# Performance work log

Measured on AMD Instinct MI355X. Metric: run time of the kernel, lower is better.

Reference implementation:

```python
import jax, jax.numpy as jnp
import numpy as np

JUMP_THRESHOLD = 0.5
BLEND = 0.7  # blend_factor in original


def _phase_corrected(x):
    # x: [B, C, T], C even; first half channels = magnitude, second = normalized phase
    half = x.shape[1] // 2
    magnitude = x[:, :half]
    phase_norm = x[:, half:]

    # phase_grad[t] = phase[t] - phase[t-1], with grad[0] = 0 (as in torch code)
    grad = jnp.concatenate(
        [jnp.zeros_like(phase_norm[:, :, :1]), phase_norm[:, :, 1:] - phase_norm[:, :, :-1]],
        axis=2,
    )
    jumps = jnp.abs(grad) > JUMP_THRESHOLD
    # The original O(T) python loop subtracts sign(grad[j]) from all positions >= j+1
    # whenever jumps[j]; equivalently a right-shifted cumulative sum of corrections.
    d = jnp.where(jumps, jnp.sign(grad), jnp.zeros_like(grad))
    corr = jnp.cumsum(d, axis=2)
    corr = jnp.concatenate([jnp.zeros_like(corr[:, :, :1]), corr[:, :, :-1]], axis=2)
    phase_smooth = phase_norm - corr

    phase = phase_smooth * (2.0 * jnp.pi) - jnp.pi

    # F.avg_pool1d(kernel=3, stride=1, padding=1) with count_include_pad=True:
    # zero-pad and divide by 3 everywhere (including edges).
    p = jnp.pad(phase, ((0, 0), (0, 0), (1, 1)))
    phase_smoothed = (p[:, :, :-2] + p[:, :, 1:-1] + p[:, :, 2:]) * (1.0 / 3.0)

    phase_final = BLEND * phase + (1.0 - BLEND) * phase_smoothed
    real_part = magnitude * jnp.cos(phase_final)
    imag_part = magnitude * jnp.sin(phase_final)
    return real_part, imag_part


def setup_inputs() -> dict:
    key = jax.random.key(0)
    x = jax.random.normal(key, (16, 128, 16384), dtype=jnp.float32)
    return {"x": x}


def reference(x):
    real_part, imag_part = _phase_corrected(x)
    return jax.lax.complex(real_part, imag_part)
```

## Files before the change

kernel.cpp:

```cpp
#include <hip/hip_runtime.h>
#include <math.h>

#define N_T   16384
#define BLOCK 1024
#define SEG   (N_T / BLOCK)
#define NWAVE (BLOCK / 64)

__device__ __forceinline__ int SW(int i) {
    return i ^ (((i >> 6) & 7) << 2);
}

template <int MODE>
__global__ __launch_bounds__(BLOCK)
void phase_kernel(const float* __restrict__ x, float* __restrict__ out) {
    __shared__ float ph[N_T];

    const int tid  = threadIdx.x;
    const int lane = tid & 63;
    const int wave = tid >> 6;
    const int r    = blockIdx.x;
    const int b    = r >> 6;
    const int c    = r & 63;
    const float* __restrict__ phase_row = x + ((size_t)(b * 128 + 64 + c)) * N_T;
    const float* __restrict__ mag_row   = x + ((size_t)(b * 128 + c)) * N_T;

    const float TWO_PI = 6.28318530717958647692f;
    const float PI_F   = 3.14159265358979323846f;
    const float THIRD  = 1.0f / 3.0f;

    #pragma unroll
    for (int i = 0; i < N_T / (BLOCK * 4); ++i) {
        int idx = (i * BLOCK + tid) * 4;
        float4 v = *reinterpret_cast<const float4*>(phase_row + idx);
        *reinterpret_cast<float4*>(&ph[SW(idx)]) = v;
    }
    __syncthreads();

    const int seg0 = tid * SEG;
    float s[SEG];
    #pragma unroll
    for (int q = 0; q < SEG / 4; ++q) {
        float4 v = *reinterpret_cast<const float4*>(&ph[SW(seg0 + q * 4)]);
        s[q * 4 + 0] = v.x; s[q * 4 + 1] = v.y;
        s[q * 4 + 2] = v.z; s[q * 4 + 3] = v.w;
    }
    float prevseg = __shfl_up(s[SEG - 1], 1);
    if (lane == 0) prevseg = (tid > 0) ? ph[SW(seg0 - 1)] : 0.0f;

    int lsum = 0;
    {
        float prev = prevseg;
        #pragma unroll
        for (int j = 0; j < SEG; ++j) {
            float g = s[j] - prev;
            if ((seg0 + j) > 0 && fabsf(g) > 0.5f) lsum += (g > 0.0f) ? 1 : -1;
            prev = s[j];
        }
    }

    int incl = lsum;
    #pragma unroll
    for (int off = 1; off < 64; off <<= 1) {
        int n = __shfl_up(incl, off);
        if (lane >= off) incl += n;
    }
    float saved;
    if (tid < NWAVE) saved = ph[tid];
    __syncthreads();
    if (lane == 63) ph[wave] = __int_as_float(incl);
    __syncthreads();
    int wpre = 0;
    #pragma unroll
    for (int w = 0; w < NWAVE; ++w) {
        int wt = __float_as_int(ph[w]);
        if (w < wave) wpre += wt;
    }
    __syncthreads();
    if (tid < NWAVE) ph[tid] = saved;
    __syncthreads();

    int running = wpre + incl - lsum;

    {
        float prev = prevseg;
        #pragma unroll
        for (int j = 0; j < SEG; ++j) {
            float cur = s[j];
            int d = 0;
            if ((seg0 + j) > 0) {
                float g = cur - prev;
                if (fabsf(g) > 0.5f) d = (g > 0.0f) ? 1 : -1;
            }
            s[j] = (cur - (float)running) * TWO_PI - PI_F;
            running += d;
            prev = cur;
        }
    }
    #pragma unroll
    for (int q = 0; q < SEG / 4; ++q) {
        *reinterpret_cast<float4*>(&ph[SW(seg0 + q * 4)]) =
            make_float4(s[q * 4 + 0], s[q * 4 + 1], s[q * 4 + 2], s[q * 4 + 3]);
    }
    __syncthreads();

    #pragma unroll
    for (int i = 0; i < N_T / (BLOCK * 4); ++i) {
        int e = (i * BLOCK + tid) * 4;
        float4 mg = *reinterpret_cast<const float4*>(mag_row + e);
        float4 pc = *reinterpret_cast<const float4*>(&ph[SW(e)]);

        float p_m1 = __shfl_up(pc.w, 1);
        if (lane == 0)  p_m1 = (e > 0) ? ph[SW(e - 1)] : 0.0f;
        float p_p4 = __shfl_down(pc.x, 1);
        if (lane == 63) p_p4 = (e + 4 < N_T) ? ph[SW(e + 4)] : 0.0f;

        float pv[6] = {p_m1, pc.x, pc.y, pc.z, pc.w, p_p4};
        float mgk[4] = {mg.x, mg.y, mg.z, mg.w};

        float re[4], im[4];
        #pragma unroll
        for (int k = 0; k < 4; ++k) {
            float sm = ((pv[k] + pv[k + 1]) + pv[k + 2]) * THIRD;
            float pf = 0.7f * pv[k + 1] + 0.3f * sm;
            float nrev = rintf(pf * 0.15915494309189535f);
            float rr = fmaf(nrev, -6.28318548202514648f, pf);
            rr = fmaf(nrev, 1.74845553e-7f, rr);
            re[k] = mgk[k] * __cosf(rr);
            if (MODE == 1) im[k] = mgk[k] * __sinf(rr);
        }
        if (MODE == 0) {
            float* orow = out + (size_t)r * N_T;
            *reinterpret_cast<float4*>(orow + e) = make_float4(re[0], re[1], re[2], re[3]);
        } else {
            float* orow = out + (size_t)r * (2 * N_T);
            *reinterpret_cast<float4*>(orow + 2 * e) =
                make_float4(re[0], im[0], re[1], im[1]);
            *reinterpret_cast<float4*>(orow + 2 * e + 4) =
                make_float4(re[2], im[2], re[3], im[3]);
        }
    }
}

extern "C" void kernel_launch(void* const* d_in, const int* in_sizes, int n_in,
                              void* d_out, int out_size, void* d_ws, size_t ws_size,
                              hipStream_t stream) {
    const float* x = (const float*)d_in[0];
    float* out = (float*)d_out;
    int n_rows = in_sizes[0] / (2 * N_T);
    if (out_size >= in_sizes[0]) {
        phase_kernel<1><<<n_rows, BLOCK, 0, stream>>>(x, out);
    } else {
        phase_kernel<0><<<n_rows, BLOCK, 0, stream>>>(x, out);
    }
}
```

Before: 39.13 us.

## Split each row's scan into chunks with a separate chunk-sum pre-pass kernel

Replaces the single 1024-thread block per row with a two-kernel decoupled scan. A first kernel counts phase jumps for each 4096-element chunk and stores the counts in workspace. The main kernel then runs 256-thread blocks per chunk, adds the counts of earlier chunks as an offset, and reconstructs the corrected boundary neighbours needed by the pooling. This gives four times as many smaller blocks for better occupancy and load balance, and it shrinks shared memory per block. The cost is a second launch and an extra full read of the phase data.

```diff
diff --git a/kernel.cpp b/kernel.cpp
--- a/kernel.cpp
+++ b/kernel.cpp
@@ -2,35 +2,84 @@
 #include <math.h>
 
 #define N_T   16384
-#define BLOCK 1024
-#define SEG   (N_T / BLOCK)
-#define NWAVE (BLOCK / 64)
+#define CHUNK 4096
+#define SEG   16
+#define CPR   4
 
 __device__ __forceinline__ int SW(int i) {
     return i ^ (((i >> 6) & 7) << 2);
 }
 
+__global__ __launch_bounds__(256)
+void chunk_sum_kernel(const float* __restrict__ x, int* __restrict__ ws) {
+    const int c    = blockIdx.x;
+    const int row  = c >> 2;
+    const int cpos = c & 3;
+    const int b    = row >> 6;
+    const int ch   = row & 63;
+    const float* __restrict__ pr =
+        x + ((size_t)(b * 128 + 64 + ch)) * N_T + cpos * CHUNK;
+    const int lane = threadIdx.x & 63;
+    const int wv   = threadIdx.x >> 6;
+    const float* __restrict__ wb = pr + wv * 1024;
+
+    float carry = 0.0f;
+    if (lane == 0 && !(cpos == 0 && wv == 0)) carry = wb[-1];
+    carry = __shfl(carry, 0);
+
+    int lsum = 0;
+    #pragma unroll
+    for (int i = 0; i < 4; ++i) {
+        float4 v = *reinterpret_cast<const float4*>(wb + i * 256 + lane * 4);
+        float up   = __shfl_up(v.w, 1);
+        float prev = (lane == 0) ? carry : up;
+        float g0 = v.x - prev;
+        float g1 = v.y - v.x;
+        float g2 = v.z - v.y;
+        float g3 = v.w - v.z;
+        bool first = (cpos == 0 && wv == 0 && i == 0 && lane == 0);
+        if (!first && fabsf(g0) > 0.5f) lsum += (g0 > 0.0f) ? 1 : -1;
+        if (fabsf(g1) > 0.5f)           lsum += (g1 > 0.0f) ? 1 : -1;
+        if (fabsf(g2) > 0.5f)           lsum += (g2 > 0.0f) ? 1 : -1;
+        if (fabsf(g3) > 0.5f)           lsum += (g3 > 0.0f) ? 1 : -1;
+        carry = __shfl(v.w, 63);
+    }
+    #pragma unroll
+    for (int off = 32; off; off >>= 1) lsum += __shfl_xor(lsum, off);
+
+    __shared__ int ws4[4];
+    if (lane == 0) ws4[wv] = lsum;
+    __syncthreads();
+    if (threadIdx.x == 0) ws[c] = ws4[0] + ws4[1] + ws4[2] + ws4[3];
+}
+
 template <int MODE>
-__global__ __launch_bounds__(BLOCK)
-void phase_kernel(const float* __restrict__ x, float* __restrict__ out) {
-    __shared__ float ph[N_T];
+__global__ __launch_bounds__(256)
+void phase_kernel(const float* __restrict__ x, float* __restrict__ out,
+                  const int* __restrict__ ws) {
+    __shared__ float ph[CHUNK];
+    __shared__ int   wsum[4];
 
     const int tid  = threadIdx.x;
     const int lane = tid & 63;
-    const int wave = tid >> 6;
-    const int r    = blockIdx.x;
-    const int b    = r >> 6;
-    const int c    = r & 63;
-    const float* __restrict__ phase_row = x + ((size_t)(b * 128 + 64 + c)) * N_T;
-    const float* __restrict__ mag_row   = x + ((size_t)(b * 128 + c)) * N_T;
+    const int wv   = tid >> 6;
+    const int c    = blockIdx.x;
+    const int row  = c >> 2;
+    const int cpos = c & 3;
+    const int b    = row >> 6;
+    const int ch   = row & 63;
+    const float* __restrict__ phase_row =
+        x + ((size_t)(b * 128 + 64 + ch)) * N_T + cpos * CHUNK;
+    const float* __restrict__ mag_row =
+        x + ((size_t)(b * 128 + ch)) * N_T + cpos * CHUNK;
 
     const float TWO_PI = 6.28318530717958647692f;
     const float PI_F   = 3.14159265358979323846f;
     const float THIRD  = 1.0f / 3.0f;
 
     #pragma unroll
-    for (int i = 0; i < N_T / (BLOCK * 4); ++i) {
-        int idx = (i * BLOCK + tid) * 4;
+    for (int i = 0; i < 4; ++i) {
+        int idx = (i * 256 + tid) * 4;
         float4 v = *reinterpret_cast<const float4*>(phase_row + idx);
         *reinterpret_cast<float4*>(&ph[SW(idx)]) = v;
     }
@@ -45,7 +94,11 @@
         s[q * 4 + 2] = v.z; s[q * 4 + 3] = v.w;
     }
     float prevseg = __shfl_up(s[SEG - 1], 1);
-    if (lane == 0) prevseg = (tid > 0) ? ph[SW(seg0 - 1)] : 0.0f;
+    if (lane == 0) {
+        if (tid > 0)            prevseg = ph[SW(seg0 - 1)];
+        else if (cpos > 0)      prevseg = phase_row[-1];
+        else                    prevseg = 0.0f;
+    }
 
     int lsum = 0;
     {
@@ -53,7 +106,8 @@
         #pragma unroll
         for (int j = 0; j < SEG; ++j) {
             float g = s[j] - prev;
-            if ((seg0 + j) > 0 && fabsf(g) > 0.5f) lsum += (g > 0.0f) ? 1 : -1;
+            bool first = (cpos == 0 && (seg0 + j) == 0);
+            if (!first && fabsf(g) > 0.5f) lsum += (g > 0.0f) ? 1 : -1;
             prev = s[j];
         }
     }
@@ -64,22 +118,18 @@
         int n = __shfl_up(incl, off);
         if (lane >= off) incl += n;
     }
-    float saved;
-    if (tid < NWAVE) saved = ph[tid];
-    __syncthreads();
-    if (lane == 63) ph[wave] = __int_as_float(incl);
+    if (lane == 63) wsum[wv] = incl;
     __syncthreads();
     int wpre = 0;
     #pragma unroll
-    for (int w = 0; w < NWAVE; ++w) {
-        int wt = __float_as_int(ph[w]);
-        if (w < wave) wpre += wt;
-    }
-    __syncthreads();
-    if (tid < NWAVE) ph[tid] = saved;
-    __syncthreads();
-
-    int running = wpre + incl - lsum;
+    for (int w = 0; w < 4; ++w) {
+        int wt = wsum[w];
+        if (w < wv) wpre += wt;
+    }
+    int P_c = 0;
+    for (int k = 0; k < cpos; ++k) P_c += ws[row * CPR + k];
+
+    int running = P_c + wpre + (incl - lsum);
 
     {
         float prev = prevseg;
@@ -87,7 +137,8 @@
         for (int j = 0; j < SEG; ++j) {
             float cur = s[j];
             int d = 0;
-            if ((seg0 + j) > 0) {
+            bool first = (cpos == 0 && (seg0 + j) == 0);
+            if (!first) {
                 float g = cur - prev;
                 if (fabsf(g) > 0.5f) d = (g > 0.0f) ? 1 : -1;
             }
@@ -101,18 +152,33 @@
         *reinterpret_cast<float4*>(&ph[SW(seg0 + q * 4)]) =
             make_float4(s[q * 4 + 0], s[q * 4 + 1], s[q * 4 + 2], s[q * 4 + 3]);
     }
-    __syncthreads();
-
-    #pragma unroll
-    for (int i = 0; i < N_T / (BLOCK * 4); ++i) {
-        int e = (i * BLOCK + tid) * 4;
+
+    float v_left = 0.0f, v_right = 0.0f;
+    if (tid == 0 && cpos > 0) {
+        float xm1 = phase_row[-1];
+        float xm2 = phase_row[-2];
+        float g = xm1 - xm2;
+        int d = (fabsf(g) > 0.5f) ? ((g > 0.0f) ? 1 : -1) : 0;
+        int corr = P_c - d;
+        v_left = (xm1 - (float)corr) * TWO_PI - PI_F;
+    }
+    if (tid == 255 && cpos < CPR - 1) {
+        float xp = phase_row[CHUNK];
+        int corr = P_c + ws[row * CPR + cpos];
+        v_right = (xp - (float)corr) * TWO_PI - PI_F;
+    }
+    __syncthreads();
+
+    #pragma unroll
+    for (int i = 0; i < 4; ++i) {
+        int e = (i * 256 + tid) * 4;
         float4 mg = *reinterpret_cast<const float4*>(mag_row + e);
         float4 pc = *reinterpret_cast<const float4*>(&ph[SW(e)]);
 
         float p_m1 = __shfl_up(pc.w, 1);
-        if (lane == 0)  p_m1 = (e > 0) ? ph[SW(e - 1)] : 0.0f;
+        if (lane == 0)  p_m1 = (e > 0) ? ph[SW(e - 1)] : v_left;
         float p_p4 = __shfl_down(pc.x, 1);
-        if (lane == 63) p_p4 = (e + 4 < N_T) ? ph[SW(e + 4)] : 0.0f;
+        if (lane == 63) p_p4 = (e + 4 < CHUNK) ? ph[SW(e + 4)] : v_right;
 
         float pv[6] = {p_m1, pc.x, pc.y, pc.z, pc.w, p_p4};
         float mgk[4] = {mg.x, mg.y, mg.z, mg.w};
@@ -129,10 +195,10 @@
             if (MODE == 1) im[k] = mgk[k] * __sinf(rr);
         }
         if (MODE == 0) {
-            float* orow = out + (size_t)r * N_T;
+            float* orow = out + (size_t)row * N_T + cpos * CHUNK;
             *reinterpret_cast<float4*>(orow + e) = make_float4(re[0], re[1], re[2], re[3]);
         } else {
-            float* orow = out + (size_t)r * (2 * N_T);
+            float* orow = out + (size_t)row * (2 * N_T) + cpos * (2 * CHUNK);
             *reinterpret_cast<float4*>(orow + 2 * e) =
                 make_float4(re[0], im[0], re[1], im[1]);
             *reinterpret_cast<float4*>(orow + 2 * e + 4) =
@@ -146,10 +212,14 @@
                               hipStream_t stream) {
     const float* x = (const float*)d_in[0];
     float* out = (float*)d_out;
-    int n_rows = in_sizes[0] / (2 * N_T);
+    int* ws = (int*)d_ws;
+    int n_rows   = in_sizes[0] / (2 * N_T);
+    int n_chunks = n_rows * CPR;
+
+    chunk_sum_kernel<<<n_chunks, 256, 0, stream>>>(x, ws);
     if (out_size >= in_sizes[0]) {
-        phase_kernel<1><<<n_rows, BLOCK, 0, stream>>>(x, out);
+        phase_kernel<1><<<n_chunks, 256, 0, stream>>>(x, out, ws);
     } else {
-        phase_kernel<0><<<n_rows, BLOCK, 0, stream>>>(x, out);
-    }
-}
+        phase_kernel<0><<<n_chunks, 256, 0, stream>>>(x, out, ws);
+    }
+}
```

Result: slower. 45.68 us (+16.7%).

## Drop shared-memory staging; load per-thread segments directly from global

Applied to the files above, without the earlier changes.

Each thread now loads its contiguous 16-element phase and magnitude segments straight from global memory into registers, replacing the 64KB shared-memory staging buffer. The smoothing stencil is computed in registers using wave shuffles plus small per-wave edge arrays in shared memory. This removes the LDS round-trips and several barriers, and lets more blocks fit per CU because LDS use drops. The cost is that global loads and stores are strided per thread (64-byte chunks per lane) rather than coalesced across lanes, which may lower memory efficiency.

```diff
diff --git a/kernel.cpp b/kernel.cpp
--- a/kernel.cpp
+++ b/kernel.cpp
@@ -3,21 +3,19 @@
 
 #define N_T   16384
 #define BLOCK 1024
-#define SEG   (N_T / BLOCK)
-#define NWAVE (BLOCK / 64)
-
-__device__ __forceinline__ int SW(int i) {
-    return i ^ (((i >> 6) & 7) << 2);
-}
+#define SEG   16
+#define NWAVE 16
 
 template <int MODE>
 __global__ __launch_bounds__(BLOCK)
 void phase_kernel(const float* __restrict__ x, float* __restrict__ out) {
-    __shared__ float ph[N_T];
+    __shared__ int   wsum[NWAVE];
+    __shared__ float wedgeL[NWAVE];
+    __shared__ float wedgeR[NWAVE];
 
     const int tid  = threadIdx.x;
     const int lane = tid & 63;
-    const int wave = tid >> 6;
+    const int wv   = tid >> 6;
     const int r    = blockIdx.x;
     const int b    = r >> 6;
     const int c    = r & 63;
@@ -28,24 +26,22 @@
     const float PI_F   = 3.14159265358979323846f;
     const float THIRD  = 1.0f / 3.0f;
 
-    #pragma unroll
-    for (int i = 0; i < N_T / (BLOCK * 4); ++i) {
-        int idx = (i * BLOCK + tid) * 4;
-        float4 v = *reinterpret_cast<const float4*>(phase_row + idx);
-        *reinterpret_cast<float4*>(&ph[SW(idx)]) = v;
-    }
-    __syncthreads();
+    const int seg0 = tid * SEG;
 
-    const int seg0 = tid * SEG;
-    float s[SEG];
-    #pragma unroll
-    for (int q = 0; q < SEG / 4; ++q) {
-        float4 v = *reinterpret_cast<const float4*>(&ph[SW(seg0 + q * 4)]);
-        s[q * 4 + 0] = v.x; s[q * 4 + 1] = v.y;
-        s[q * 4 + 2] = v.z; s[q * 4 + 3] = v.w;
-    }
+    float4 p0 = *reinterpret_cast<const float4*>(phase_row + seg0);
+    float4 p1 = *reinterpret_cast<const float4*>(phase_row + seg0 + 4);
+    float4 p2 = *reinterpret_cast<const float4*>(phase_row + seg0 + 8);
+    float4 p3 = *reinterpret_cast<const float4*>(phase_row + seg0 + 12);
+    float4 m0 = *reinterpret_cast<const float4*>(mag_row + seg0);
+    float4 m1 = *reinterpret_cast<const float4*>(mag_row + seg0 + 4);
+    float4 m2 = *reinterpret_cast<const float4*>(mag_row + seg0 + 8);
+    float4 m3 = *reinterpret_cast<const float4*>(mag_row + seg0 + 12);
+
+    float s[SEG] = {p0.x, p0.y, p0.z, p0.w, p1.x, p1.y, p1.z, p1.w,
+                    p2.x, p2.y, p2.z, p2.w, p3.x, p3.y, p3.z, p3.w};
+
     float prevseg = __shfl_up(s[SEG - 1], 1);
-    if (lane == 0) prevseg = (tid > 0) ? ph[SW(seg0 - 1)] : 0.0f;
+    if (lane == 0) prevseg = (tid > 0) ? phase_row[seg0 - 1] : 0.0f;
 
     int lsum = 0;
     {
@@ -64,21 +60,14 @@
         int n = __shfl_up(incl, off);
         if (lane >= off) incl += n;
     }
-    float saved;
-    if (tid < NWAVE) saved = ph[tid];
-    __syncthreads();
-    if (lane == 63) ph[wave] = __int_as_float(incl);
+    if (lane == 63) wsum[wv] = incl;
     __syncthreads();
     int wpre = 0;
     #pragma unroll
     for (int w = 0; w < NWAVE; ++w) {
-        int wt = __float_as_int(ph[w]);
-        if (w < wave) wpre += wt;
+        int wt = wsum[w];
+        if (w < wv) wpre += wt;
     }
-    __syncthreads();
-    if (tid < NWAVE) ph[tid] = saved;
-    __syncthreads();
-
     int running = wpre + incl - lsum;
 
     {
@@ -96,48 +85,42 @@
             prev = cur;
         }
     }
+
+    if (lane == 0)  wedgeL[wv] = s[0];
+    if (lane == 63) wedgeR[wv] = s[SEG - 1];
+    __syncthreads();
+    float left = __shfl_up(s[SEG - 1], 1);
+    if (lane == 0)  left  = (wv > 0)     ? wedgeR[wv - 1] : 0.0f;
+    float right = __shfl_down(s[0], 1);
+    if (lane == 63) right = (wv < NWAVE - 1) ? wedgeL[wv + 1] : 0.0f;
+
+    float mgk[SEG] = {m0.x, m0.y, m0.z, m0.w, m1.x, m1.y, m1.z, m1.w,
+                      m2.x, m2.y, m2.z, m2.w, m3.x, m3.y, m3.z, m3.w};
+    float re[SEG], im[SEG];
     #pragma unroll
-    for (int q = 0; q < SEG / 4; ++q) {
-        *reinterpret_cast<float4*>(&ph[SW(seg0 + q * 4)]) =
-            make_float4(s[q * 4 + 0], s[q * 4 + 1], s[q * 4 + 2], s[q * 4 + 3]);
+    for (int j = 0; j < SEG; ++j) {
+        float pm = (j == 0)       ? left  : s[j - 1];
+        float pp = (j == SEG - 1) ? right : s[j + 1];
+        float sm = ((pm + s[j]) + pp) * THIRD;
+        float pf = 0.7f * s[j] + 0.3f * sm;
+        float nrev = rintf(pf * 0.15915494309189535f);
+        float rr = fmaf(nrev, -6.28318548202514648f, pf);
+        rr = fmaf(nrev, 1.74845553e-7f, rr);
+        re[j] = mgk[j] * __cosf(rr);
+        if (MODE == 1) im[j] = mgk[j] * __sinf(rr);
     }
-    __syncthreads();
-
-    #pragma unroll
-    for (int i = 0; i < N_T / (BLOCK * 4); ++i) {
-        int e = (i * BLOCK + tid) * 4;
-        float4 mg = *reinterpret_cast<const float4*>(mag_row + e);
-        float4 pc = *reinterpret_cast<const float4*>(&ph[SW(e)]);
-
-        float p_m1 = __shfl_up(pc.w, 1);
-        if (lane == 0)  p_m1 = (e > 0) ? ph[SW(e - 1)] : 0.0f;
-        float p_p4 = __shfl_down(pc.x, 1);
-        if (lane == 63) p_p4 = (e + 4 < N_T) ? ph[SW(e + 4)] : 0.0f;
-
-        float pv[6] = {p_m1, pc.x, pc.y, pc.z, pc.w, p_p4};
-        float mgk[4] = {mg.x, mg.y, mg.z, mg.w};
-
-        float re[4], im[4];
+    if (MODE == 0) {
+        float* o = out + (size_t)r * N_T + seg0;
         #pragma unroll
-        for (int k = 0; k < 4; ++k) {
-            float sm = ((pv[k] + pv[k + 1]) + pv[k + 2]) * THIRD;
-            float pf = 0.7f * pv[k + 1] + 0.3f * sm;
-            float nrev = rintf(pf * 0.15915494309189535f);
-            float rr = fmaf(nrev, -6.28318548202514648f, pf);
-            rr = fmaf(nrev, 1.74845553e-7f, rr);
-            re[k] = mgk[k] * __cosf(rr);
-            if (MODE == 1) im[k] = mgk[k] * __sinf(rr);
-        }
-        if (MODE == 0) {
-            float* orow = out + (size_t)r * N_T;
-            *reinterpret_cast<float4*>(orow + e) = make_float4(re[0], re[1], re[2], re[3]);
-        } else {
-            float* orow = out + (size_t)r * (2 * N_T);
-            *reinterpret_cast<float4*>(orow + 2 * e) =
-                make_float4(re[0], im[0], re[1], im[1]);
-            *reinterpret_cast<float4*>(orow + 2 * e + 4) =
-                make_float4(re[2], im[2], re[3], im[3]);
-        }
+        for (int q = 0; q < SEG / 4; ++q)
+            *reinterpret_cast<float4*>(o + q * 4) =
+                make_float4(re[q*4], re[q*4+1], re[q*4+2], re[q*4+3]);
+    } else {
+        float* o = out + (size_t)r * (2 * N_T) + 2 * seg0;
+        #pragma unroll
+        for (int q = 0; q < SEG / 2; ++q)
+            *reinterpret_cast<float4*>(o + q * 4) =
+                make_float4(re[q*2], im[q*2], re[q*2+1], im[q*2+1]);
     }
 }
 
```

Result: slower. 50.96 us (+30.2%).

## Replace 64KB LDS row staging with register-resident chunked scan

Applied to the files above, without the earlier changes.

Each thread now keeps its phase values in registers, four strided chunks of four, instead of staging the whole 16K row in shared memory and re-reading it with a swizzle. The scan becomes a per-chunk wave scan plus small shared arrays that carry the wave totals and boundary values. The magnitude loads are issued before the final barrier. This drops the 64KB LDS footprint, which should allow more blocks per CU and remove the LDS round trips, at the cost of more shuffles and more complex boundary handling.

```diff
diff --git a/kernel.cpp b/kernel.cpp
--- a/kernel.cpp
+++ b/kernel.cpp
@@ -1,23 +1,23 @@
 #include <hip/hip_runtime.h>
 #include <math.h>
 
-#define N_T   16384
-#define BLOCK 1024
-#define SEG   (N_T / BLOCK)
-#define NWAVE (BLOCK / 64)
-
-__device__ __forceinline__ int SW(int i) {
-    return i ^ (((i >> 6) & 7) << 2);
-}
+#define N_T    16384
+#define BLOCK  1024
+#define NCH    4
+#define CHSZ   4096
+#define NWAVE  16
 
 template <int MODE>
 __global__ __launch_bounds__(BLOCK)
 void phase_kernel(const float* __restrict__ x, float* __restrict__ out) {
-    __shared__ float ph[N_T];
+    __shared__ float rawEdge[NCH][NWAVE];
+    __shared__ int   wtot[NCH][NWAVE];
+    __shared__ float corrR[NCH][NWAVE];
+    __shared__ float corrL[NCH][NWAVE];
 
     const int tid  = threadIdx.x;
     const int lane = tid & 63;
-    const int wave = tid >> 6;
+    const int wv   = tid >> 6;
     const int r    = blockIdx.x;
     const int b    = r >> 6;
     const int c    = r & 63;
@@ -28,100 +28,137 @@
     const float PI_F   = 3.14159265358979323846f;
     const float THIRD  = 1.0f / 3.0f;
 
+    float s[16];
     #pragma unroll
-    for (int i = 0; i < N_T / (BLOCK * 4); ++i) {
-        int idx = (i * BLOCK + tid) * 4;
-        float4 v = *reinterpret_cast<const float4*>(phase_row + idx);
-        *reinterpret_cast<float4*>(&ph[SW(idx)]) = v;
+    for (int i = 0; i < NCH; ++i) {
+        float4 v = *reinterpret_cast<const float4*>(phase_row + i * CHSZ + tid * 4);
+        s[i * 4 + 0] = v.x; s[i * 4 + 1] = v.y;
+        s[i * 4 + 2] = v.z; s[i * 4 + 3] = v.w;
+    }
+
+    if (lane == 63) {
+        #pragma unroll
+        for (int i = 0; i < NCH; ++i) rawEdge[i][wv] = s[i * 4 + 3];
     }
     __syncthreads();
 
-    const int seg0 = tid * SEG;
-    float s[SEG];
+    float prevRaw[NCH];
     #pragma unroll
-    for (int q = 0; q < SEG / 4; ++q) {
-        float4 v = *reinterpret_cast<const float4*>(&ph[SW(seg0 + q * 4)]);
-        s[q * 4 + 0] = v.x; s[q * 4 + 1] = v.y;
-        s[q * 4 + 2] = v.z; s[q * 4 + 3] = v.w;
+    for (int i = 0; i < NCH; ++i) {
+        float p = __shfl_up(s[i * 4 + 3], 1);
+        if (lane == 0) {
+            if (wv > 0)      p = rawEdge[i][wv - 1];
+            else if (i > 0)  p = rawEdge[i - 1][NWAVE - 1];
+            else             p = 0.0f;
+        }
+        prevRaw[i] = p;
     }
-    float prevseg = __shfl_up(s[SEG - 1], 1);
-    if (lane == 0) prevseg = (tid > 0) ? ph[SW(seg0 - 1)] : 0.0f;
 
-    int lsum = 0;
+    int lsum[NCH];
+    #pragma unroll
+    for (int i = 0; i < NCH; ++i) {
+        float prev = prevRaw[i];
+        int cnt = 0;
+        #pragma unroll
+        for (int k = 0; k < 4; ++k) {
+            float cur = s[i * 4 + k];
+            float g = cur - prev;
+            bool first = (i == 0 && tid == 0 && k == 0);
+            if (!first && fabsf(g) > 0.5f) cnt += (g > 0.0f) ? 1 : -1;
+            prev = cur;
+        }
+        lsum[i] = cnt;
+    }
+
+    int incl[NCH] = {lsum[0], lsum[1], lsum[2], lsum[3]};
+    #pragma unroll
+    for (int off = 1; off < 64; off <<= 1) {
+        #pragma unroll
+        for (int i = 0; i < NCH; ++i) {
+            int n = __shfl_up(incl[i], off);
+            if (lane >= off) incl[i] += n;
+        }
+    }
+    if (lane == 63) {
+        #pragma unroll
+        for (int i = 0; i < NCH; ++i) wtot[i][wv] = incl[i];
+    }
+    __syncthreads();
+
+    int P[NCH];
     {
-        float prev = prevseg;
+        int chunkPre = 0;
         #pragma unroll
-        for (int j = 0; j < SEG; ++j) {
-            float g = s[j] - prev;
-            if ((seg0 + j) > 0 && fabsf(g) > 0.5f) lsum += (g > 0.0f) ? 1 : -1;
-            prev = s[j];
+        for (int i = 0; i < NCH; ++i) {
+            int wpre = 0, tot = 0;
+            #pragma unroll
+            for (int w = 0; w < NWAVE; ++w) {
+                int t = wtot[i][w];
+                if (w < wv) wpre += t;
+                tot += t;
+            }
+            P[i] = chunkPre + wpre + (incl[i] - lsum[i]);
+            chunkPre += tot;
         }
     }
 
-    int incl = lsum;
     #pragma unroll
-    for (int off = 1; off < 64; off <<= 1) {
-        int n = __shfl_up(incl, off);
-        if (lane >= off) incl += n;
-    }
-    float saved;
-    if (tid < NWAVE) saved = ph[tid];
-    __syncthreads();
-    if (lane == 63) ph[wave] = __int_as_float(incl);
-    __syncthreads();
-    int wpre = 0;
-    #pragma unroll
-    for (int w = 0; w < NWAVE; ++w) {
-        int wt = __float_as_int(ph[w]);
-        if (w < wave) wpre += wt;
-    }
-    __syncthreads();
-    if (tid < NWAVE) ph[tid] = saved;
-    __syncthreads();
-
-    int running = wpre + incl - lsum;
-
-    {
-        float prev = prevseg;
+    for (int i = 0; i < NCH; ++i) {
+        int running = P[i];
+        float prev = prevRaw[i];
         #pragma unroll
-        for (int j = 0; j < SEG; ++j) {
-            float cur = s[j];
+        for (int k = 0; k < 4; ++k) {
+            float cur = s[i * 4 + k];
             int d = 0;
-            if ((seg0 + j) > 0) {
+            bool first = (i == 0 && tid == 0 && k == 0);
+            if (!first) {
                 float g = cur - prev;
                 if (fabsf(g) > 0.5f) d = (g > 0.0f) ? 1 : -1;
             }
-            s[j] = (cur - (float)running) * TWO_PI - PI_F;
+            s[i * 4 + k] = (cur - (float)running) * TWO_PI - PI_F;
             running += d;
             prev = cur;
         }
     }
+
+    if (lane == 63) {
+        #pragma unroll
+        for (int i = 0; i < NCH; ++i) corrR[i][wv] = s[i * 4 + 3];
+    }
+    if (lane == 0) {
+        #pragma unroll
+        for (int i = 0; i < NCH; ++i) corrL[i][wv] = s[i * 4 + 0];
+    }
+    float4 mg[NCH];
     #pragma unroll
-    for (int q = 0; q < SEG / 4; ++q) {
-        *reinterpret_cast<float4*>(&ph[SW(seg0 + q * 4)]) =
-            make_float4(s[q * 4 + 0], s[q * 4 + 1], s[q * 4 + 2], s[q * 4 + 3]);
-    }
+    for (int i = 0; i < NCH; ++i)
+        mg[i] = *reinterpret_cast<const float4*>(mag_row + i * CHSZ + tid * 4);
     __syncthreads();
 
     #pragma unroll
-    for (int i = 0; i < N_T / (BLOCK * 4); ++i) {
-        int e = (i * BLOCK + tid) * 4;
-        float4 mg = *reinterpret_cast<const float4*>(mag_row + e);
-        float4 pc = *reinterpret_cast<const float4*>(&ph[SW(e)]);
+    for (int i = 0; i < NCH; ++i) {
+        float left = __shfl_up(s[i * 4 + 3], 1);
+        if (lane == 0) {
+            if (wv > 0)      left = corrR[i][wv - 1];
+            else if (i > 0)  left = corrR[i - 1][NWAVE - 1];
+            else             left = 0.0f;
+        }
+        float right = __shfl_down(s[i * 4 + 0], 1);
+        if (lane == 63) {
+            if (wv < NWAVE - 1)  right = corrL[i][wv + 1];
+            else if (i < NCH - 1) right = corrL[i + 1][0];
+            else                  right = 0.0f;
+        }
 
-        float p_m1 = __shfl_up(pc.w, 1);
-        if (lane == 0)  p_m1 = (e > 0) ? ph[SW(e - 1)] : 0.0f;
-        float p_p4 = __shfl_down(pc.x, 1);
-        if (lane == 63) p_p4 = (e + 4 < N_T) ? ph[SW(e + 4)] : 0.0f;
-
-        float pv[6] = {p_m1, pc.x, pc.y, pc.z, pc.w, p_p4};
-        float mgk[4] = {mg.x, mg.y, mg.z, mg.w};
-
+        float mgk[4] = {mg[i].x, mg[i].y, mg[i].z, mg[i].w};
         float re[4], im[4];
         #pragma unroll
         for (int k = 0; k < 4; ++k) {
-            float sm = ((pv[k] + pv[k + 1]) + pv[k + 2]) * THIRD;
-            float pf = 0.7f * pv[k + 1] + 0.3f * sm;
+            float pm = (k == 0) ? left  : s[i * 4 + k - 1];
+            float pp = (k == 3) ? right : s[i * 4 + k + 1];
+            float cur = s[i * 4 + k];
+            float sm = ((pm + cur) + pp) * THIRD;
+            float pf = 0.7f * cur + 0.3f * sm;
             float nrev = rintf(pf * 0.15915494309189535f);
             float rr = fmaf(nrev, -6.28318548202514648f, pf);
             rr = fmaf(nrev, 1.74845553e-7f, rr);
@@ -129,14 +166,12 @@
             if (MODE == 1) im[k] = mgk[k] * __sinf(rr);
         }
         if (MODE == 0) {
-            float* orow = out + (size_t)r * N_T;
-            *reinterpret_cast<float4*>(orow + e) = make_float4(re[0], re[1], re[2], re[3]);
+            float* o = out + (size_t)r * N_T + i * CHSZ + tid * 4;
+            *reinterpret_cast<float4*>(o) = make_float4(re[0], re[1], re[2], re[3]);
         } else {
-            float* orow = out + (size_t)r * (2 * N_T);
-            *reinterpret_cast<float4*>(orow + 2 * e) =
-                make_float4(re[0], im[0], re[1], im[1]);
-            *reinterpret_cast<float4*>(orow + 2 * e + 4) =
-                make_float4(re[2], im[2], re[3], im[3]);
+            float* o = out + (size_t)r * (2 * N_T) + 2 * (i * CHSZ + tid * 4);
+            *reinterpret_cast<float4*>(o)     = make_float4(re[0], im[0], re[1], im[1]);
+            *reinterpret_cast<float4*>(o + 4) = make_float4(re[2], im[2], re[3], im[3]);
         }
     }
 }
```

After: 36.05 us. -7.9%, faster.
